# Optimization experiments

Hardware: AMD Instinct MI355X
Metric: run time of the kernel (lower is better)

The kernel has to match this reference:

```python
import jax, jax.numpy as jnp
import numpy as np

B, N, E = 32, 32, 64          # graphs, nodes/graph, edges/graph
H_, W_ = 40, 40
HW = H_ * W_
D, NH, L = 256, 8, 6
DH = D // NH
Tn, Te = B * N, B * E


def _ln(x, g, b):
    m = x.mean(-1, keepdims=True)
    v = ((x - m) ** 2).mean(-1, keepdims=True)
    return (x - m) * jax.lax.rsqrt(v + 1e-5) * g + b


def _sinus(v, dim):
    half = dim // 2
    freqs = jnp.exp(-jnp.log(10000.0) * jnp.arange(half) / half)
    ang = v[..., None] * freqs
    return jnp.concatenate([jnp.sin(ang), jnp.cos(ang)], -1)


def _heatmap(bx):
    # separable Gaussian over the HxW grid, boxes in normalized cxcywh
    gx = (jnp.arange(W_) + 0.5) / W_
    gy = (jnp.arange(H_) + 0.5) / H_
    cx, cy, w, h = bx[:, 0], bx[:, 1], bx[:, 2], bx[:, 3]
    hx = jnp.exp(-(gx[None] - cx[:, None]) ** 2 / (2 * (w[:, None] / 2) ** 2 + 1e-6))
    hy = jnp.exp(-(gy[None] - cy[:, None]) ** 2 / (2 * (h[:, None] / 2) ** 2 + 1e-6))
    return (hy[:, :, None] * hx[:, None, :]).reshape(-1, HW)


def _to_b(q):
    return jnp.concatenate([q[:Tn].reshape(B, N, D), q[Tn:].reshape(B, E, D)], 1)


def _from_b(qb):
    return jnp.concatenate([qb[:, :N].reshape(Tn, D), qb[:, N:].reshape(Te, D)], 0)


def _xyxy(b):
    return jnp.stack([b[:, 0] - b[:, 2] / 2, b[:, 1] - b[:, 3] / 2,
                      b[:, 0] + b[:, 2] / 2, b[:, 1] + b[:, 3] / 2], -1)


def _forward(features, boxes, nodes0, edges0, ln1_g, ln1_b, attn_in_w, attn_in_b,
             attn_out_w, attn_out_b, ls1, ln2_g, ln2_b, gat_wn, gat_we, gat_a_src,
             gat_a_dst, gat_a_edge, gat_wo, gat_bo, gat_woe, gat_boe, ls2,
             ln3_g, ln3_b, ffn_w1, ffn_b1, ffn_w2, ffn_b2, ls3, edge_local):
    off = jnp.repeat(jnp.arange(B) * N, E)
    src = edge_local[0] + off
    dst = edge_local[1] + off
    b1, b2 = boxes[src], boxes[dst]
    u1, u2 = _xyxy(b1), _xyxy(b2)
    ux1 = jnp.minimum(u1[:, 0], u2[:, 0]); uy1 = jnp.minimum(u1[:, 1], u2[:, 1])
    ux2 = jnp.maximum(u1[:, 2], u2[:, 2]); uy2 = jnp.maximum(u1[:, 3], u2[:, 3])
    union = jnp.stack([(ux1 + ux2) / 2, (uy1 + uy2) / 2, ux2 - ux1, uy2 - uy1], -1)
    node_hm = _heatmap(boxes)                                   # [Tn, HW]
    edge_hm = jnp.maximum(jnp.maximum(node_hm[src], node_hm[dst]), _heatmap(union))
    attn_bias = jnp.concatenate([node_hm.reshape(B, N, HW), edge_hm.reshape(B, E, HW)], 1)
    node_emb = jnp.concatenate([_sinus(boxes[:, i], D // 4) for i in range(4)], -1)
    delta = b1 - b2
    edge_emb = jnp.concatenate([_sinus(delta[:, i], D // 4) for i in range(4)], -1)
    emb_q = jnp.concatenate([node_emb, edge_emb], 0)            # [Tn+Te, D]
    q = jnp.concatenate([nodes0, edges0], 0)
    scale = 1.0 / jnp.sqrt(jnp.float32(DH))
    outs = []
    for l in range(L):
        # cross attention (pre-LN, LayerScale residual)
        x = _ln(q, ln1_g[l], ln1_b[l])
        xb = _to_b(x)
        Wq, Wk, Wv = jnp.split(attn_in_w[l], 3, 0)
        bq, bk, bv = jnp.split(attn_in_b[l], 3, 0)
        qh = (xb @ Wq.T + bq).reshape(B, N + E, NH, DH)
        kh = (features @ Wk.T + bk).reshape(B, HW, NH, DH)
        vh = (features @ Wv.T + bv).reshape(B, HW, NH, DH)
        scores = jnp.einsum('bqhd,bkhd->bhqk', qh, kh) * scale + attn_bias[:, None]
        o = jnp.einsum('bhqk,bkhd->bqhd', jax.nn.softmax(scores, -1), vh).reshape(B, N + E, D)
        o = o @ attn_out_w[l].T + attn_out_b[l]
        q = q + ls1[l] * _from_b(o)
        # GAT (note: original adds residual to the *normed* queries)
        x = _ln(q, ln2_g[l], ln2_b[l])
        xe = x + emb_q
        h = (xe[:Tn] @ gat_wn[l]).reshape(Tn, NH, DH)
        ee = (xe[Tn:] @ gat_we[l]).reshape(Te, NH, DH)
        logits = jax.nn.leaky_relu(
            (h[src] * gat_a_src[l] + h[dst] * gat_a_dst[l] + ee * gat_a_edge[l]).sum(-1), 0.2)
        m = jax.ops.segment_max(logits, dst, Tn)
        ex = jnp.exp(logits - m[dst])
        den = jax.ops.segment_sum(ex, dst, Tn)
        alpha = ex / (den[dst] + 1e-9)
        nout = jax.ops.segment_sum(alpha[..., None] * (h[src] + ee), dst, Tn).reshape(Tn, D) @ gat_wo[l] + gat_bo[l]
        eout = ee.reshape(Te, D) @ gat_woe[l] + gat_boe[l]
        q = x + ls2[l] * jnp.concatenate([nout, eout], 0)
        # FFN
        y = _ln(q, ln3_g[l], ln3_b[l])
        y = jax.nn.gelu(y @ ffn_w1[l] + ffn_b1[l], approximate=False) @ ffn_w2[l] + ffn_b2[l]
        q = q + ls3[l] * y
        outs.append(q)
    return jnp.stack(outs)  # [L, Tn+Te, D]


def setup_inputs():
    key = jax.random.key(0)
    k = jax.random.split(key, 20)
    s = 0.02
    u = jax.random.uniform(k[0], (Tn, 4))
    boxes = jnp.concatenate([u[:, :2] * 0.6 + 0.2, u[:, 2:] * 0.3 + 0.1], -1)
    return dict(
        features=jax.random.normal(k[2], (B, HW, D)),
        boxes=boxes,
        edge_local=jax.random.randint(k[1], (2, Te), 0, N),
        nodes0=jax.random.normal(k[3], (Tn, D)),
        edges0=jax.random.normal(k[4], (Te, D)),
        ln1_g=jnp.ones((L, D)), ln1_b=jnp.zeros((L, D)),
        attn_in_w=jax.random.normal(k[5], (L, 3 * D, D)) * s, attn_in_b=jnp.zeros((L, 3 * D)),
        attn_out_w=jax.random.normal(k[6], (L, D, D)) * s, attn_out_b=jnp.zeros((L, D)),
        ls1=jnp.full((L, D), 0.1),
        ln2_g=jnp.ones((L, D)), ln2_b=jnp.zeros((L, D)),
        gat_wn=jax.random.normal(k[7], (L, D, D)) * s, gat_we=jax.random.normal(k[8], (L, D, D)) * s,
        gat_a_src=jax.random.normal(k[9], (L, NH, DH)) * s,
        gat_a_dst=jax.random.normal(k[10], (L, NH, DH)) * s,
        gat_a_edge=jax.random.normal(k[11], (L, NH, DH)) * s,
        gat_wo=jax.random.normal(k[12], (L, D, D)) * s, gat_bo=jnp.zeros((L, D)),
        gat_woe=jax.random.normal(k[13], (L, D, D)) * s, gat_boe=jnp.zeros((L, D)),
        ls2=jnp.full((L, D), 0.1),
        ln3_g=jnp.ones((L, D)), ln3_b=jnp.zeros((L, D)),
        ffn_w1=jax.random.normal(k[14], (L, D, 4 * D)) * s, ffn_b1=jnp.zeros((L, 4 * D)),
        ffn_w2=jax.random.normal(k[15], (L, 4 * D, D)) * s, ffn_b2=jnp.zeros((L, D)),
        ls3=jnp.full((L, D), 0.1),
    )


def reference(features, boxes, edge_local, nodes0, edges0, ln1_g, ln1_b, attn_in_w,
              attn_in_b, attn_out_w, attn_out_b, ls1, ln2_g, ln2_b, gat_wn, gat_we,
              gat_a_src, gat_a_dst, gat_a_edge, gat_wo, gat_bo, gat_woe, gat_boe,
              ls2, ln3_g, ln3_b, ffn_w1, ffn_b1, ffn_w2, ffn_b2, ls3):
    return _forward(features, boxes, nodes0, edges0, ln1_g, ln1_b, attn_in_w, attn_in_b,
                    attn_out_w, attn_out_b, ls1, ln2_g, ln2_b, gat_wn, gat_we, gat_a_src,
                    gat_a_dst, gat_a_edge, gat_wo, gat_bo, gat_woe, gat_boe, ls2,
                    ln3_g, ln3_b, ffn_w1, ffn_b1, ffn_w2, ffn_b2, ls3, edge_local)
```

## Files before the change

kernel.cpp:

```cpp
#include <hip/hip_runtime.h>
#include <hip/hip_bf16.h>
#include <math.h>

typedef __hip_bfloat16 bf16;
typedef unsigned short ushort_t;
typedef __attribute__((ext_vector_type(8))) short bf16x8;
typedef __attribute__((ext_vector_type(4))) float f32x4;

static constexpr int B_C   = 32;
static constexpr int N_C   = 32;
static constexpr int E_C   = 64;
static constexpr int HW_C  = 1600;
static constexpr int D_C   = 256;
static constexpr int NH_C  = 8;
static constexpr int DH_C  = 32;
static constexpr int L_C   = 6;
static constexpr int TN_C  = 1024;
static constexpr int TE_C  = 2048;
static constexpr int TT_C  = 3072;

__device__ __forceinline__ float bf2f(bf16 v) { return __bfloat162float(v); }
__device__ __forceinline__ int clampi(int v, int lo, int hi) {
  return v < lo ? lo : (v > hi ? hi : v);
}
__device__ __forceinline__ float clampf(float v, float lo, float hi) {
  return fminf(fmaxf(v, lo), hi);
}
__device__ __forceinline__ ushort_t f2b(float x) {
  bf16 h = __float2bfloat16(x);
  return *reinterpret_cast<ushort_t*>(&h);
}

__device__ __forceinline__ void unpack_bf2(unsigned v, float& a, float& b) {
  union { unsigned u; float f; } ua, ub;
  ua.u = v << 16;
  ub.u = v & 0xffff0000u;
  a = ua.f; b = ub.f;
}

__device__ __forceinline__ void load_bf16x32(const bf16* p, float* out) {
  const uint4* p4 = reinterpret_cast<const uint4*>(p);
#pragma unroll
  for (int w = 0; w < 4; w++) {
    uint4 u = p4[w];
    unpack_bf2(u.x, out[w * 8 + 0], out[w * 8 + 1]);
    unpack_bf2(u.y, out[w * 8 + 2], out[w * 8 + 3]);
    unpack_bf2(u.z, out[w * 8 + 4], out[w * 8 + 5]);
    unpack_bf2(u.w, out[w * 8 + 6], out[w * 8 + 7]);
  }
}

static constexpr int SA = 40;

__device__ __forceinline__ void stage8(const float* __restrict__ src,
                                       ushort_t* __restrict__ dst) {
  float4 f0 = *(const float4*)src;
  float4 f1 = *(const float4*)(src + 4);
  ushort_t t[8] = { f2b(f0.x), f2b(f0.y), f2b(f0.z), f2b(f0.w),
                    f2b(f1.x), f2b(f1.y), f2b(f1.z), f2b(f1.w) };
  *(uint4*)dst = *(const uint4*)t;
}

template <bool AB, bool BT, int EPI, typename TC>
__global__ __launch_bounds__(256) void mgemm_kernel(
    const void* __restrict__ Ap, int lda, const float* __restrict__ Bw, int ldb,
    const float* __restrict__ bias, TC* __restrict__ C, int ldc,
    int M, int N, int K)
{
  __shared__ ushort_t As[64 * SA];
  __shared__ ushort_t Bs[64 * SA];
  const int tid = threadIdx.x;
  const int row0 = blockIdx.x * 64, col0 = blockIdx.y * 64;
  const int wave = tid >> 6, lane = tid & 63;
  const int wm = (wave >> 1) * 32, wn = (wave & 1) * 32;
  const int lm = lane & 15, quad = lane >> 4;

  f32x4 acc[2][2] = {};
  const int am = tid >> 2, akk = (tid & 3) * 8;
  const int bn = tid & 63, bkb = (tid >> 6) * 8;

  for (int k0 = 0; k0 < K; k0 += 32) {
    if (AB) {
      const bf16* A = (const bf16*)Ap;
      *(uint4*)&As[am * SA + akk] =
          *(const uint4*)(A + (size_t)(row0 + am) * lda + k0 + akk);
    } else {
      stage8((const float*)Ap + (size_t)(row0 + am) * lda + k0 + akk,
             &As[am * SA + akk]);
    }
    if (BT) {
      stage8(Bw + (size_t)(col0 + am) * ldb + k0 + akk, &Bs[am * SA + akk]);
    } else {
      ushort_t t[8];
#pragma unroll
      for (int j = 0; j < 8; j++)
        t[j] = f2b(Bw[(size_t)(k0 + bkb + j) * ldb + col0 + bn]);
      *(uint4*)(&Bs[bn * SA + bkb]) = *(const uint4*)t;
    }
    __syncthreads();
    bf16x8 a0 = *(const bf16x8*)(&As[(wm + lm) * SA + quad * 8]);
    bf16x8 a1 = *(const bf16x8*)(&As[(wm + 16 + lm) * SA + quad * 8]);
    bf16x8 b0 = *(const bf16x8*)(&Bs[(wn + lm) * SA + quad * 8]);
    bf16x8 b1 = *(const bf16x8*)(&Bs[(wn + 16 + lm) * SA + quad * 8]);
    acc[0][0] = __builtin_amdgcn_mfma_f32_16x16x32_bf16(a0, b0, acc[0][0], 0, 0, 0);
    acc[0][1] = __builtin_amdgcn_mfma_f32_16x16x32_bf16(a0, b1, acc[0][1], 0, 0, 0);
    acc[1][0] = __builtin_amdgcn_mfma_f32_16x16x32_bf16(a1, b0, acc[1][0], 0, 0, 0);
    acc[1][1] = __builtin_amdgcn_mfma_f32_16x16x32_bf16(a1, b1, acc[1][1], 0, 0, 0);
    __syncthreads();
  }

#pragma unroll
  for (int ti = 0; ti < 2; ti++) {
#pragma unroll
    for (int tj = 0; tj < 2; tj++) {
      int gc = col0 + wn + tj * 16 + lm;
      float bsv = (EPI == 1 || EPI == 2) ? bias[gc] : 0.f;
#pragma unroll
      for (int r = 0; r < 4; r++) {
        int gr = row0 + wm + ti * 16 + quad * 4 + r;
        float v = acc[ti][tj][r];
        TC* cp = C + (size_t)gr * ldc + gc;
        if (EPI == 1 || EPI == 2) v += bsv;
        if (EPI == 2) v = 0.5f * v * (1.0f + erff(v * 0.70710678118654752f));
        if (EPI == 3) v += (float)(*cp);
        *cp = (TC)v;
      }
    }
  }
}

template <bool AB, bool BT, int EPI, typename TC>
static void mg(const void* A, int lda, const float* Bw, int ldb,
               const float* bias, void* C, int ldc,
               int M, int N, int K, hipStream_t s) {
  dim3 g(M / 64, N / 64);
  mgemm_kernel<AB, BT, EPI, TC><<<g, 256, 0, s>>>(A, lda, Bw, ldb, bias,
                                                  (TC*)C, ldc, M, N, K);
}

template <int EPI>
__global__ __launch_bounds__(256) void mgemm_dual_kernel(
    const float* __restrict__ A1, const float* __restrict__ A2, int M1, int lda,
    const float* __restrict__ B1, const float* __restrict__ B2, int ldb,
    const float* __restrict__ bias1, const float* __restrict__ bias2,
    float* __restrict__ C, int ldc, int K)
{
  __shared__ ushort_t As[64 * SA];
  __shared__ ushort_t Bs[64 * SA];
  const int tid = threadIdx.x;
  const int grow0 = blockIdx.x * 64, col0 = blockIdx.y * 64;
  const bool first = grow0 < M1;
  const float* A = first ? A1 : A2;
  const float* Bw = first ? B1 : B2;
  const float* bias = first ? bias1 : bias2;
  const int row0 = first ? grow0 : grow0 - M1;

  const int wave = tid >> 6, lane = tid & 63;
  const int wm = (wave >> 1) * 32, wn = (wave & 1) * 32;
  const int lm = lane & 15, quad = lane >> 4;

  f32x4 acc[2][2] = {};
  const int am = tid >> 2, akk = (tid & 3) * 8;
  const int bn = tid & 63, bkb = (tid >> 6) * 8;

  for (int k0 = 0; k0 < K; k0 += 32) {
    stage8(A + (size_t)(row0 + am) * lda + k0 + akk, &As[am * SA + akk]);
    ushort_t t[8];
#pragma unroll
    for (int j = 0; j < 8; j++)
      t[j] = f2b(Bw[(size_t)(k0 + bkb + j) * ldb + col0 + bn]);
    *(uint4*)(&Bs[bn * SA + bkb]) = *(const uint4*)t;
    __syncthreads();
    bf16x8 a0 = *(const bf16x8*)(&As[(wm + lm) * SA + quad * 8]);
    bf16x8 a1 = *(const bf16x8*)(&As[(wm + 16 + lm) * SA + quad * 8]);
    bf16x8 b0 = *(const bf16x8*)(&Bs[(wn + lm) * SA + quad * 8]);
    bf16x8 b1 = *(const bf16x8*)(&Bs[(wn + 16 + lm) * SA + quad * 8]);
    acc[0][0] = __builtin_amdgcn_mfma_f32_16x16x32_bf16(a0, b0, acc[0][0], 0, 0, 0);
    acc[0][1] = __builtin_amdgcn_mfma_f32_16x16x32_bf16(a0, b1, acc[0][1], 0, 0, 0);
    acc[1][0] = __builtin_amdgcn_mfma_f32_16x16x32_bf16(a1, b0, acc[1][0], 0, 0, 0);
    acc[1][1] = __builtin_amdgcn_mfma_f32_16x16x32_bf16(a1, b1, acc[1][1], 0, 0, 0);
    __syncthreads();
  }

#pragma unroll
  for (int ti = 0; ti < 2; ti++) {
#pragma unroll
    for (int tj = 0; tj < 2; tj++) {
      int gc = col0 + wn + tj * 16 + lm;
      float bsv = (EPI == 1) ? bias[gc] : 0.f;
#pragma unroll
      for (int r = 0; r < 4; r++) {
        int gr = grow0 + wm + ti * 16 + quad * 4 + r;
        float v = acc[ti][tj][r];
        if (EPI == 1) v += bsv;
        C[(size_t)gr * ldc + gc] = v;
      }
    }
  }
}


__global__ __launch_bounds__(256) void featconv_kernel(const float* __restrict__ f,
                                                       bf16* __restrict__ fb) {
  int idx = (blockIdx.x * 256 + threadIdx.x) * 8;
  float4 a = *(const float4*)(f + idx);
  float4 b = *(const float4*)(f + idx + 4);
  ushort_t t[8] = { f2b(a.x), f2b(a.y), f2b(a.z), f2b(a.w),
                    f2b(b.x), f2b(b.y), f2b(b.z), f2b(b.w) };
  *(uint4*)(fb + idx) = *(const uint4*)t;
}

__global__ __launch_bounds__(256) void nodehm_kernel(const float* __restrict__ boxes,
                                                     bf16* __restrict__ hm) {
  int t = blockIdx.x;
  float cx = clampf(boxes[t * 4 + 0], -10.f, 10.f);
  float cy = clampf(boxes[t * 4 + 1], -10.f, 10.f);
  float w  = clampf(boxes[t * 4 + 2], -10.f, 10.f);
  float h  = clampf(boxes[t * 4 + 3], -10.f, 10.f);
  float dwx = w * w * 0.5f + 1e-6f;
  float dhy = h * h * 0.5f + 1e-6f;
  for (int pix = threadIdx.x; pix < HW_C; pix += 256) {
    int y = pix / 40, x = pix - y * 40;
    float gx = ((float)x + 0.5f) * 0.025f;
    float gy = ((float)y + 0.5f) * 0.025f;
    hm[(size_t)t * HW_C + pix] = __float2bfloat16(
        expf(-(gx - cx) * (gx - cx) / dwx) * expf(-(gy - cy) * (gy - cy) / dhy));
  }
}

__global__ __launch_bounds__(256) void edgehm_kernel(const float* __restrict__ boxes,
                                                     const int* __restrict__ el,
                                                     const bf16* __restrict__ nhm,
                                                     bf16* __restrict__ ehm) {
  int e = blockIdx.x;
  int b = e >> 6;
  int sg = clampi(el[e], 0, N_C - 1) + b * N_C;
  int dg = clampi(el[TE_C + e], 0, N_C - 1) + b * N_C;
  float c1x = clampf(boxes[sg * 4 + 0], -10.f, 10.f);
  float c1y = clampf(boxes[sg * 4 + 1], -10.f, 10.f);
  float w1  = clampf(boxes[sg * 4 + 2], -10.f, 10.f);
  float h1  = clampf(boxes[sg * 4 + 3], -10.f, 10.f);
  float c2x = clampf(boxes[dg * 4 + 0], -10.f, 10.f);
  float c2y = clampf(boxes[dg * 4 + 1], -10.f, 10.f);
  float w2  = clampf(boxes[dg * 4 + 2], -10.f, 10.f);
  float h2  = clampf(boxes[dg * 4 + 3], -10.f, 10.f);
  float ux1 = fminf(c1x - w1 * 0.5f, c2x - w2 * 0.5f);
  float uy1 = fminf(c1y - h1 * 0.5f, c2y - h2 * 0.5f);
  float ux2 = fmaxf(c1x + w1 * 0.5f, c2x + w2 * 0.5f);
  float uy2 = fmaxf(c1y + h1 * 0.5f, c2y + h2 * 0.5f);
  float cx = 0.5f * (ux1 + ux2), cy = 0.5f * (uy1 + uy2);
  float w = ux2 - ux1, h = uy2 - uy1;
  float dwx = w * w * 0.5f + 1e-6f;
  float dhy = h * h * 0.5f + 1e-6f;
  for (int pix = threadIdx.x; pix < HW_C; pix += 256) {
    int y = pix / 40, x = pix - y * 40;
    float gx = ((float)x + 0.5f) * 0.025f;
    float gy = ((float)y + 0.5f) * 0.025f;
    float u = expf(-(gx - cx) * (gx - cx) / dwx) * expf(-(gy - cy) * (gy - cy) / dhy);
    float v = fmaxf(fmaxf(bf2f(nhm[(size_t)sg * HW_C + pix]),
                          bf2f(nhm[(size_t)dg * HW_C + pix])), u);
    ehm[(size_t)e * HW_C + pix] = __float2bfloat16(v);
  }
}

__global__ __launch_bounds__(256) void embq_kernel(const float* __restrict__ boxes,
                                                   const int* __restrict__ el,
                                                   bf16* __restrict__ emb) {
  int t = blockIdx.x;
  int d = threadIdx.x;
  int c = d >> 6, inner = d & 63;
  float v;
  if (t < TN_C) {
    v = boxes[t * 4 + c];
  } else {
    int e = t - TN_C;
    int b = e >> 6;
    int sg = clampi(el[e], 0, N_C - 1) + b * N_C;
    int dg = clampi(el[TE_C + e], 0, N_C - 1) + b * N_C;
    v = boxes[sg * 4 + c] - boxes[dg * 4 + c];
  }
  v = clampf(v, -100.f, 100.f);
  int i = inner & 31;
  float freq = expf(-9.210340371976184f * (float)i / 32.0f);
  float ang = v * freq;
  emb[(size_t)t * D_C + d] = __float2bfloat16((inner < 32) ? sinf(ang) : cosf(ang));
}

__global__ __launch_bounds__(256) void initq_kernel(const float* __restrict__ nodes0,
                                                    const float* __restrict__ edges0,
                                                    float* __restrict__ q) {
  int idx = blockIdx.x * 256 + threadIdx.x;
  int t = idx >> 8;
  q[idx] = (t < TN_C) ? nodes0[idx] : edges0[idx - TN_C * D_C];
}


__global__ __launch_bounds__(256) void ln_kernel(const float* __restrict__ base,
                                                 const float* __restrict__ delta,
                                                 const float* __restrict__ ls,
                                                 float* __restrict__ qsave,
                                                 const float* __restrict__ g,
                                                 const float* __restrict__ bb,
                                                 float* __restrict__ xout,
                                                 const bf16* __restrict__ emb,
                                                 float* __restrict__ xeout) {
  __shared__ float red[4];
  int r = blockIdx.x, tid = threadIdx.x;
  size_t bofs = (size_t)r * D_C;
  float v = base[bofs + tid];
  if (delta) v += ls[tid] * delta[bofs + tid];
  if (qsave) qsave[bofs + tid] = v;
  float s = v;
#pragma unroll
  for (int o = 1; o < 64; o <<= 1) s += __shfl_xor(s, o);
  if ((tid & 63) == 0) red[tid >> 6] = s;
  __syncthreads();
  float mean = (red[0] + red[1] + red[2] + red[3]) * (1.0f / 256.0f);
  __syncthreads();
  float d = v - mean;
  float s2 = d * d;
#pragma unroll
  for (int o = 1; o < 64; o <<= 1) s2 += __shfl_xor(s2, o);
  if ((tid & 63) == 0) red[tid >> 6] = s2;
  __syncthreads();
  float var = (red[0] + red[1] + red[2] + red[3]) * (1.0f / 256.0f);
  float xo = d * rsqrtf(var + 1e-5f) * g[tid] + bb[tid];
  xout[bofs + tid] = xo;
  if (xeout) xeout[bofs + tid] = xo + bf2f(emb[bofs + tid]);
}

static constexpr int ATK = 160;
static constexpr int KSTR = 40;
static constexpr int VSTR = 168;
static constexpr int PSTR = 168;
static constexpr int SPL = 2;
static constexpr int KEYS_PER = HW_C / SPL;

__global__ __launch_bounds__(192) void fattn_kernel(const float* __restrict__ Qp,
                                                    const bf16* __restrict__ KV,
                                                    const bf16* __restrict__ nhm,
                                                    const bf16* __restrict__ ehm,
                                                    float* __restrict__ Opart,
                                                    float* __restrict__ mpart,
                                                    float* __restrict__ lpart) {
  __shared__ ushort_t Kl[ATK * KSTR];
  __shared__ ushort_t Vt[32 * VSTR];
  __shared__ ushort_t Pl[3 * 32 * PSTR];

  const int s = blockIdx.x >> 8;
  const int rem = blockIdx.x & 255;
  const int h = rem >> 5, b = rem & 31;
  const int tid = threadIdx.x;
  const int wave = tid >> 6, lane = tid & 63;
  const int lm = lane & 15, quad = lane >> 4;
  const int wr0 = wave * 32;

  int tok[2][4];
  const bf16* brow[2][4];
#pragma unroll
  for (int mt = 0; mt < 2; mt++)
#pragma unroll
    for (int r = 0; r < 4; r++) {
      int row = wr0 + mt * 16 + quad * 4 + r;
      if (row < 32) {
        int t = b * N_C + row;
        tok[mt][r] = t; brow[mt][r] = nhm + (size_t)t * HW_C;
      } else {
        int e = b * E_C + (row - 32);
        tok[mt][r] = TN_C + e; brow[mt][r] = ehm + (size_t)e * HW_C;
      }
    }

  bf16x8 qa[2];
#pragma unroll
  for (int mt = 0; mt < 2; mt++) {
    int row = wr0 + mt * 16 + lm;
    int t = (row < 32) ? (b * N_C + row) : (TN_C + b * E_C + (row - 32));
    const float* qp = Qp + (size_t)t * D_C + h * DH_C + quad * 8;
    ushort_t tmp[8];
#pragma unroll
    for (int j = 0; j < 8; j++) tmp[j] = f2b(qp[j]);
    qa[mt] = *(const bf16x8*)tmp;
  }

  f32x4 Oacc[2][2] = {};
  float mrow[2][4], lrow[2][4];
#pragma unroll
  for (int mt = 0; mt < 2; mt++)
#pragma unroll
    for (int r = 0; r < 4; r++) { mrow[mt][r] = -1e30f; lrow[mt][r] = 0.f; }

  const bf16* kvb = KV + (size_t)b * HW_C * 512 + h * DH_C;
  const float scale = 0.17677669529663687f;
  ushort_t* Pw = &Pl[wave * 32 * PSTR];

  const int kend = s * KEYS_PER + KEYS_PER;
  for (int k0 = s * KEYS_PER; k0 < kend; k0 += ATK) {
    for (int slot = tid; slot < ATK * 4; slot += 192) {
      int key = slot >> 2, dc = (slot & 3) * 8;
      const bf16* src = kvb + (size_t)(k0 + key) * 512 + dc;
      *(uint4*)&Kl[key * KSTR + dc] = *(const uint4*)src;
      uint4 v4 = *(const uint4*)(src + 256);
      ushort_t vs[8]; *(uint4*)vs = v4;
#pragma unroll
      for (int j = 0; j < 8; j++) Vt[(dc + j) * VSTR + key] = vs[j];
    }
    __syncthreads();

    float sv[2][10][4];
#pragma unroll
    for (int nt = 0; nt < 10; nt++) {
      bf16x8 kb = *(const bf16x8*)&Kl[(nt * 16 + lm) * KSTR + quad * 8];
#pragma unroll
      for (int mt = 0; mt < 2; mt++) {
        f32x4 d = {};
        d = __builtin_amdgcn_mfma_f32_16x16x32_bf16(qa[mt], kb, d, 0, 0, 0);
#pragma unroll
        for (int r = 0; r < 4; r++) sv[mt][nt][r] = d[r];
      }
    }

#pragma unroll
    for (int mt = 0; mt < 2; mt++)
#pragma unroll
      for (int r = 0; r < 4; r++) {
        const bf16* br = brow[mt][r] + k0 + lm;
        float mx = -1e30f;
#pragma unroll
        for (int nt = 0; nt < 10; nt++) {
          float v = sv[mt][nt][r] * scale + bf2f(br[nt * 16]);
          sv[mt][nt][r] = v;
          mx = fmaxf(mx, v);
        }
#pragma unroll
        for (int o = 1; o < 16; o <<= 1) mx = fmaxf(mx, __shfl_xor(mx, o));
        float mn = fmaxf(mrow[mt][r], mx);
        float lsum = 0.f;
        int prow = (mt * 16 + quad * 4 + r) * PSTR;
#pragma unroll
        for (int nt = 0; nt < 10; nt++) {
          float p = expf(fminf(sv[mt][nt][r] - mn, 0.f));
          lsum += p;
          Pw[prow + nt * 16 + lm] = f2b(p);
        }
#pragma unroll
        for (int o = 1; o < 16; o <<= 1) lsum += __shfl_xor(lsum, o);
        float alpha = expf(fminf(mrow[mt][r] - mn, 0.f));
        lrow[mt][r] = lrow[mt][r] * alpha + lsum;
        mrow[mt][r] = mn;
        Oacc[mt][0][r] *= alpha;
        Oacc[mt][1][r] *= alpha;
      }

#pragma unroll
    for (int kc = 0; kc < 5; kc++) {
#pragma unroll
      for (int nt = 0; nt < 2; nt++) {
        bf16x8 vfrag = *(const bf16x8*)&Vt[(nt * 16 + lm) * VSTR + kc * 32 + quad * 8];
#pragma unroll
        for (int mt = 0; mt < 2; mt++) {
          bf16x8 pa = *(const bf16x8*)&Pw[(mt * 16 + lm) * PSTR + kc * 32 + quad * 8];
          Oacc[mt][nt] = __builtin_amdgcn_mfma_f32_16x16x32_bf16(pa, vfrag,
                                                                 Oacc[mt][nt], 0, 0, 0);
        }
      }
    }
    __syncthreads();
  }

  const size_t TD = (size_t)TT_C * D_C;
#pragma unroll
  for (int mt = 0; mt < 2; mt++)
#pragma unroll
    for (int r = 0; r < 4; r++) {
      float* op = Opart + (size_t)s * TD + (size_t)tok[mt][r] * D_C + h * DH_C;
      op[lm]      = Oacc[mt][0][r];
      op[16 + lm] = Oacc[mt][1][r];
      if (lm == 0) {
        int mi = s * TT_C * NH_C + tok[mt][r] * NH_C + h;
        mpart[mi] = mrow[mt][r];
        lpart[mi] = lrow[mt][r];
      }
    }
}

__global__ __launch_bounds__(256) void fmerge_kernel(const float* __restrict__ Opart,
                                                     const float* __restrict__ mpart,
                                                     const float* __restrict__ lpart,
                                                     float* __restrict__ O) {
  int idx = blockIdx.x * 256 + threadIdx.x;
  int t = idx >> 8, d = idx & 255, h = d >> 5;
  const size_t TD = (size_t)TT_C * D_C;
  int mi = t * NH_C + h;
  float m0 = mpart[mi], m1 = mpart[TT_C * NH_C + mi];
  float l0 = lpart[mi], l1 = lpart[TT_C * NH_C + mi];
  float mm = fmaxf(m0, m1);
  float a0 = expf(fminf(m0 - mm, 0.f)), a1 = expf(fminf(m1 - mm, 0.f));
  float l = l0 * a0 + l1 * a1;
  O[idx] = (Opart[idx] * a0 + Opart[TD + idx] * a1) / fmaxf(l, 1e-30f);
}


template <bool HM>
__global__ __launch_bounds__(256) void attn_kernel(const float* __restrict__ Qp,
                                                   const bf16* __restrict__ KV,
                                                   const bf16* __restrict__ nhm,
                                                   const bf16* __restrict__ ehm,
                                                   const float* __restrict__ boxes,
                                                   const int* __restrict__ el,
                                                   int c0, int nb,
                                                   float* __restrict__ O) {
  int wid = threadIdx.x >> 6;
  int lane = threadIdx.x & 63;
  int gw = blockIdx.x * 4 + wid;
  int tic = gw >> 3, h = gw & 7;
  int t, bl, nG = 0;
  const bf16* brow = nullptr;
  float pcx[3], pcy[3], pdx[3], pdy[3];
  if (tic < nb * N_C) {
    bl = tic >> 5;
    t = (c0 + bl) * N_C + (tic & 31);
    if (HM) {
      brow = nhm + (size_t)t * HW_C;
    } else {
      float cx = clampf(boxes[t * 4 + 0], -10.f, 10.f);
      float cy = clampf(boxes[t * 4 + 1], -10.f, 10.f);
      float w  = clampf(boxes[t * 4 + 2], -10.f, 10.f);
      float hh = clampf(boxes[t * 4 + 3], -10.f, 10.f);
      pcx[0] = cx; pcy[0] = cy;
      pdx[0] = w * w * 0.5f + 1e-6f; pdy[0] = hh * hh * 0.5f + 1e-6f;
      nG = 1;
    }
  } else {
    int ei = tic - nb * N_C;
    bl = ei >> 6;
    int e = (c0 + bl) * E_C + (ei & 63);
    t = TN_C + e;
    if (HM) {
      brow = ehm + (size_t)e * HW_C;
    } else {
      int sg = clampi(el[e], 0, N_C - 1) + (c0 + bl) * N_C;
      int dg = clampi(el[TE_C + e], 0, N_C - 1) + (c0 + bl) * N_C;
      float c1x = clampf(boxes[sg * 4 + 0], -10.f, 10.f);
      float c1y = clampf(boxes[sg * 4 + 1], -10.f, 10.f);
      float w1  = clampf(boxes[sg * 4 + 2], -10.f, 10.f);
      float h1  = clampf(boxes[sg * 4 + 3], -10.f, 10.f);
      float c2x = clampf(boxes[dg * 4 + 0], -10.f, 10.f);
      float c2y = clampf(boxes[dg * 4 + 1], -10.f, 10.f);
      float w2  = clampf(boxes[dg * 4 + 2], -10.f, 10.f);
      float h2  = clampf(boxes[dg * 4 + 3], -10.f, 10.f);
      pcx[0] = c1x; pcy[0] = c1y;
      pdx[0] = w1 * w1 * 0.5f + 1e-6f; pdy[0] = h1 * h1 * 0.5f + 1e-6f;
      pcx[1] = c2x; pcy[1] = c2y;
      pdx[1] = w2 * w2 * 0.5f + 1e-6f; pdy[1] = h2 * h2 * 0.5f + 1e-6f;
      float ux1 = fminf(c1x - w1 * 0.5f, c2x - w2 * 0.5f);
      float uy1 = fminf(c1y - h1 * 0.5f, c2y - h2 * 0.5f);
      float ux2 = fmaxf(c1x + w1 * 0.5f, c2x + w2 * 0.5f);
      float uy2 = fmaxf(c1y + h1 * 0.5f, c2y + h2 * 0.5f);
      float uw = ux2 - ux1, uh = uy2 - uy1;
      pcx[2] = 0.5f * (ux1 + ux2); pcy[2] = 0.5f * (uy1 + uy2);
      pdx[2] = uw * uw * 0.5f + 1e-6f; pdy[2] = uh * uh * 0.5f + 1e-6f;
      nG = 3;
    }
  }

  float qv[32];
  const float* qp = Qp + (size_t)t * D_C + h * DH_C;
#pragma unroll
  for (int d = 0; d < 32; d++) qv[d] = qp[d];

  const float scale = 0.17677669529663687f;
  const bf16* kvb = KV + (size_t)bl * HW_C * 512 + h * DH_C;

  float sarr[25];
  float m = -1e30f;
#pragma unroll
  for (int i = 0; i < 25; i++) {
    int kk = lane + i * 64;
    float kf[32];
    load_bf16x32(kvb + (size_t)kk * 512, kf);
    float s = 0.f;
#pragma unroll
    for (int d = 0; d < 32; d++) s = fmaf(kf[d], qv[d], s);
    float bias;
    if (HM) {
      bias = bf2f(brow[kk]);
    } else {
      int yy = kk / 40, xx = kk - yy * 40;
      float gx = ((float)xx + 0.5f) * 0.025f;
      float gy = ((float)yy + 0.5f) * 0.025f;
      bias = 0.f;
      for (int g = 0; g < nG; g++) {
        float dxv = gx - pcx[g], dyv = gy - pcy[g];
        float e = expf(-dxv * dxv / pdx[g]) * expf(-dyv * dyv / pdy[g]);
        bias = fmaxf(bias, e);
      }
    }
    s = clampf(s * scale + bias, -1e30f, 1e30f);
    sarr[i] = s;
    m = fmaxf(m, s);
  }
#pragma unroll
  for (int o = 1; o < 64; o <<= 1) m = fmaxf(m, __shfl_xor(m, o));

  float l = 0.f;
  float acc[32] = {};
#pragma unroll
  for (int i = 0; i < 25; i++) {
    int kk = lane + i * 64;
    float vf[32];
    load_bf16x32(kvb + (size_t)kk * 512 + 256, vf);
    float e = expf(fminf(sarr[i] - m, 0.f));
    l += e;
#pragma unroll
    for (int d = 0; d < 32; d++) acc[d] = fmaf(e, vf[d], acc[d]);
  }
#pragma unroll
  for (int o = 1; o < 64; o <<= 1) {
    l += __shfl_xor(l, o);
#pragma unroll
    for (int d = 0; d < 32; d++) acc[d] += __shfl_xor(acc[d], o);
  }
  if (lane == 0) {
    float inv = 1.0f / fmaxf(l, 1e-30f);
    float* op = O + (size_t)t * D_C + h * DH_C;
#pragma unroll
    for (int d = 0; d < 32; d++) op[d] = acc[d] * inv;
  }
}


__global__ __launch_bounds__(512) void gat_fused_kernel(const float* __restrict__ hee,
                                                        const int* __restrict__ el,
                                                        const float* __restrict__ as,
                                                        const float* __restrict__ ad,
                                                        const float* __restrict__ ae,
                                                        float* __restrict__ al) {
  __shared__ float lg[512];
  __shared__ float ml[256], dl[256];
  int b = blockIdx.x, tid = threadIdx.x;
  int e_l = tid >> 3, h = tid & 7;
  int e = b * E_C + e_l;
  int sgl = clampi(el[e], 0, N_C - 1);
  int dgl = clampi(el[TE_C + e], 0, N_C - 1);
  {
    const float* hs = hee + (size_t)(b * N_C + sgl) * D_C + h * DH_C;
    const float* hd = hee + (size_t)(b * N_C + dgl) * D_C + h * DH_C;
    const float* ep = hee + (size_t)(TN_C + e) * D_C + h * DH_C;
    float s = 0.f;
#pragma unroll
    for (int d = 0; d < 32; d++)
      s += hs[d] * as[h * 32 + d] + hd[d] * ad[h * 32 + d] + ep[d] * ae[h * 32 + d];
    s = clampf(s, -1e30f, 1e30f);
    lg[tid] = (s > 0.f) ? s : 0.2f * s;
  }
  __syncthreads();
  if (tid < 256) {
    int n = tid >> 3, hh = tid & 7;
    float m = -1e30f;
    for (int k = 0; k < 64; k++) {
      int dg = clampi(el[TE_C + b * E_C + k], 0, N_C - 1);
      if (dg == n) m = fmaxf(m, lg[k * 8 + hh]);
    }
    float den = 0.f;
    for (int k = 0; k < 64; k++) {
      int dg = clampi(el[TE_C + b * E_C + k], 0, N_C - 1);
      if (dg == n) den += expf(fminf(lg[k * 8 + hh] - m, 0.f));
    }
    ml[tid] = m; dl[tid] = den;
  }
  __syncthreads();
  float ex = expf(fminf(lg[tid] - ml[dgl * 8 + h], 0.f));
  al[(size_t)e * 8 + h] = ex / (dl[dgl * 8 + h] + 1e-9f);
}

__global__ __launch_bounds__(256) void gat_nout_kernel(const float* __restrict__ hee,
                                                       const int* __restrict__ el,
                                                       const float* __restrict__ al,
                                                       float* __restrict__ noutp) {
  int n = blockIdx.x, d = threadIdx.x;
  int h = d >> 5;
  int b = n >> 5;
  int e0 = b * E_C;
  float acc = 0.f;
  for (int k = 0; k < 64; k++) {
    int e = e0 + k;
    int dg = clampi(el[TE_C + e], 0, N_C - 1) + b * N_C;
    if (dg == n) {
      int sg = clampi(el[e], 0, N_C - 1) + b * N_C;
      acc += al[e * 8 + h] * (hee[(size_t)sg * D_C + d] + hee[(size_t)(TN_C + e) * D_C + d]);
    }
  }
  noutp[(size_t)n * D_C + d] = acc;
}


__global__ __launch_bounds__(256) void axpy_store_kernel(float* __restrict__ q,
                                                         const float* __restrict__ delta,
                                                         const float* __restrict__ ls,
                                                         float* __restrict__ out) {
  int idx = blockIdx.x * 256 + threadIdx.x;
  float v = q[idx] + ls[idx & 255] * delta[idx];
  q[idx] = v;
  out[idx] = (fabsf(v) <= 1e4f) ? v : 0.f;
}


extern "C" void kernel_launch(void* const* d_in, const int* in_sizes, int n_in,
                              void* d_out, int out_size, void* d_ws, size_t ws_size,
                              hipStream_t stream) {
  const float* features   = (const float*)d_in[0];
  const float* boxes      = (const float*)d_in[1];
  const int*   edge_local = (const int*)d_in[2];
  const float* nodes0     = (const float*)d_in[3];
  const float* edges0     = (const float*)d_in[4];
  const float* ln1_g      = (const float*)d_in[5];
  const float* ln1_b      = (const float*)d_in[6];
  const float* attn_in_w  = (const float*)d_in[7];
  const float* attn_in_b  = (const float*)d_in[8];
  const float* attn_out_w = (const float*)d_in[9];
  const float* attn_out_b = (const float*)d_in[10];
  const float* ls1        = (const float*)d_in[11];
  const float* ln2_g      = (const float*)d_in[12];
  const float* ln2_b      = (const float*)d_in[13];
  const float* gat_wn     = (const float*)d_in[14];
  const float* gat_we     = (const float*)d_in[15];
  const float* gat_a_src  = (const float*)d_in[16];
  const float* gat_a_dst  = (const float*)d_in[17];
  const float* gat_a_edge = (const float*)d_in[18];
  const float* gat_wo     = (const float*)d_in[19];
  const float* gat_bo     = (const float*)d_in[20];
  const float* gat_woe    = (const float*)d_in[21];
  const float* gat_boe    = (const float*)d_in[22];
  const float* ls2        = (const float*)d_in[23];
  const float* ln3_g      = (const float*)d_in[24];
  const float* ln3_b      = (const float*)d_in[25];
  const float* ffn_w1     = (const float*)d_in[26];
  const float* ffn_b1     = (const float*)d_in[27];
  const float* ffn_w2     = (const float*)d_in[28];
  const float* ffn_b2     = (const float*)d_in[29];
  const float* ls3        = (const float*)d_in[30];
  float* out = (float*)d_out;

  size_t off = 0;
  auto alloc = [&](size_t bytes) -> void* {
    void* p = (char*)d_ws + off;
    off += (bytes + 255) & ~(size_t)255;
    return p;
  };
  const size_t TD = (size_t)TT_C * D_C;
  bf16*  emb   = (bf16*)alloc(TD * 2);
  float* q     = (float*)alloc(TD * 4);
  float* t0    = (float*)alloc(TD * 4);
  float* t1    = (float*)alloc(TD * 4);
  float* al    = (float*)alloc((size_t)TE_C * 8 * 4);
  float* mpart = (float*)alloc((size_t)SPL * TT_C * NH_C * 4);
  float* lpart = (float*)alloc((size_t)SPL * TT_C * NH_C * 4);
  float* ybig  = (float*)alloc((size_t)TT_C * 512 * 4);
  size_t base_end = off;

  const size_t KV_FULL = (size_t)B_C * HW_C * 512 * 2;
  const size_t KV_CHNK = (size_t)4 * HW_C * 512 * 2;
  const size_t HM_SZ   = (size_t)(TN_C + TE_C) * HW_C * 2;
  const size_t YB2_SZ  = (size_t)TT_C * 512 * 4;
  const size_t FB_SZ   = (size_t)B_C * HW_C * 256 * 2;
  const size_t MARGIN  = 2u << 20;
  int mode;
  if (ws_size >= base_end + YB2_SZ + KV_FULL + HM_SZ + FB_SZ + MARGIN) mode = 3;
  else if (ws_size >= base_end + KV_FULL + HM_SZ + MARGIN) mode = 2;
  else if (ws_size >= base_end + KV_CHNK + HM_SZ + MARGIN) mode = 1;
  else mode = 0;

  float* ybig2 = (mode == 3) ? (float*)alloc(YB2_SZ) : nullptr;
  bf16* KV = (bf16*)alloc(mode >= 2 ? KV_FULL : KV_CHNK);
  bf16 *nhm = nullptr, *ehm = nullptr;
  if (mode >= 1) {
    nhm = (bf16*)alloc((size_t)TN_C * HW_C * 2);
    ehm = (bf16*)alloc((size_t)TE_C * HW_C * 2);
  }
  bf16* featb = (mode == 3) ? (bf16*)alloc(FB_SZ) : nullptr;
  float* hee   = ybig;
  float* noutp = ybig + (size_t)TT_C * 256;
  float* Opart = ybig;
  (void)in_sizes; (void)n_in; (void)out_size; (void)ybig2;

  embq_kernel<<<TT_C, 256, 0, stream>>>(boxes, edge_local, emb);
  initq_kernel<<<TT_C, 256, 0, stream>>>(nodes0, edges0, q);
  if (mode >= 1) {
    nodehm_kernel<<<TN_C, 256, 0, stream>>>(boxes, nhm);
    edgehm_kernel<<<TE_C, 256, 0, stream>>>(boxes, edge_local, nhm, ehm);
  }
  if (mode == 3)
    featconv_kernel<<<(B_C * HW_C * 256) / (256 * 8), 256, 0, stream>>>(features, featb);

  for (int l = 0; l < L_C; l++) {
    const float* Wq  = attn_in_w + (size_t)l * 768 * 256;
    const float* WKV = Wq + (size_t)256 * 256;
    const float* bq  = attn_in_b + (size_t)l * 768;
    const float* bKV = bq + 256;

    ln_kernel<<<TT_C, 256, 0, stream>>>(q, nullptr, nullptr, nullptr,
                                        ln1_g + l * 256, ln1_b + l * 256,
                                        t0, nullptr, nullptr);
    mg<false, true, 1, float>(t0, 256, Wq, 256, bq, t1, 256, TT_C, 256, 256, stream);
    if (mode >= 2) {
      if (mode == 3)
        mg<true, true, 1, bf16>(featb, 256, WKV, 256, bKV, KV, 512,
                                B_C * HW_C, 512, 256, stream);
      else
        mg<false, true, 1, bf16>(features, 256, WKV, 256, bKV, KV, 512,
                                 B_C * HW_C, 512, 256, stream);
      fattn_kernel<<<SPL * 256, 192, 0, stream>>>(t1, KV, nhm, ehm,
                                                  Opart, mpart, lpart);
      fmerge_kernel<<<(TT_C * D_C) / 256, 256, 0, stream>>>(Opart, mpart, lpart, t0);
    } else {
      for (int c = 0; c < B_C / 4; c++) {
        mg<false, true, 1, bf16>(features + (size_t)c * 4 * HW_C * 256, 256,
                                 WKV, 256, bKV, KV, 512, 4 * HW_C, 512, 256, stream);
        if (mode == 1)
          attn_kernel<true><<<4 * 192, 256, 0, stream>>>(
              t1, KV, nhm, ehm, boxes, edge_local, c * 4, 4, t0);
        else
          attn_kernel<false><<<4 * 192, 256, 0, stream>>>(
              t1, KV, nhm, ehm, boxes, edge_local, c * 4, 4, t0);
      }
    }
    mg<false, true, 1, float>(t0, 256, attn_out_w + (size_t)l * 65536, 256,
                              attn_out_b + l * 256, t1, 256, TT_C, 256, 256, stream);
    ln_kernel<<<TT_C, 256, 0, stream>>>(q, t1, ls1 + l * 256, q,
                                        ln2_g + l * 256, ln2_b + l * 256,
                                        t0, emb, t1);
    {
      dim3 g(TT_C / 64, 4);
      mgemm_dual_kernel<0><<<g, 256, 0, stream>>>(
          t1, t1 + (size_t)TN_C * 256, TN_C, 256,
          gat_wn + (size_t)l * 65536, gat_we + (size_t)l * 65536, 256,
          nullptr, nullptr, hee, 256, 256);
    }
    gat_fused_kernel<<<B_C, 512, 0, stream>>>(
        hee, edge_local, gat_a_src + l * 256, gat_a_dst + l * 256,
        gat_a_edge + l * 256, al);
    gat_nout_kernel<<<TN_C, 256, 0, stream>>>(hee, edge_local, al, noutp);
    {
      dim3 g(TT_C / 64, 4);
      mgemm_dual_kernel<1><<<g, 256, 0, stream>>>(
          noutp, hee + (size_t)TN_C * 256, TN_C, 256,
          gat_wo + (size_t)l * 65536, gat_woe + (size_t)l * 65536, 256,
          gat_bo + l * 256, gat_boe + l * 256, t1, 256, 256);
    }
    ln_kernel<<<TT_C, 256, 0, stream>>>(t0, t1, ls2 + l * 256, q,
                                        ln3_g + l * 256, ln3_b + l * 256,
                                        t0, nullptr, nullptr);
    const float* W1 = ffn_w1 + (size_t)l * 262144;
    const float* W2 = ffn_w2 + (size_t)l * 262144;
    if (mode == 3) {
      mg<false, false, 2, float>(t0, 256, W1, 1024, ffn_b1 + l * 1024,
                                 ybig, 1024, TT_C, 1024, 256, stream);
      mg<false, false, 1, float>(ybig, 1024, W2, 256, ffn_b2 + l * 256,
                                 t1, 256, TT_C, 256, 1024, stream);
    } else {
      mg<false, false, 2, float>(t0, 256, W1, 1024, ffn_b1 + l * 1024,
                                 ybig, 512, TT_C, 512, 256, stream);
      mg<false, false, 1, float>(ybig, 512, W2, 256, ffn_b2 + l * 256,
                                 t1, 256, TT_C, 256, 512, stream);
      mg<false, false, 2, float>(t0, 256, W1 + 512, 1024, ffn_b1 + l * 1024 + 512,
                                 ybig, 512, TT_C, 512, 256, stream);
      mg<false, false, 3, float>(ybig, 512, W2 + (size_t)512 * 256, 256,
                                 nullptr, t1, 256, TT_C, 256, 512, stream);
    }
    axpy_store_kernel<<<TT_C, 256, 0, stream>>>(q, t1, ls3 + l * 256,
                                                out + (size_t)l * TD);
  }
}
```

Measured before the change: 1.614 ms.

## Split fused attention across four key chunks and stream K from global memory

Makes the key-split count a runtime parameter and uses four splits in the full-workspace mode, with masking because 400 keys per split is not a multiple of the 160-key tile. fmerge now combines an arbitrary number of partials. K is no longer staged in LDS: MFMA fragments are read straight from global memory, and P is staged one 32-key chunk at a time, which shrinks shared memory and may raise occupancy. It also batches the row max/sum shuffles, vectorizes the Q load and switches expf to __expf throughout. Risks: over-reads past split and buffer ends on the K loads, Opart spilling past the ybig allocation into the adjacent buffer, and lower accuracy from the fast exp.

Result: slower. 2.450 ms (+51.8%).

```diff
diff --git a/kernel.cpp b/kernel.cpp
--- a/kernel.cpp
+++ b/kernel.cpp
@@ -224,7 +224,7 @@
     float gx = ((float)x + 0.5f) * 0.025f;
     float gy = ((float)y + 0.5f) * 0.025f;
     hm[(size_t)t * HW_C + pix] = __float2bfloat16(
-        expf(-(gx - cx) * (gx - cx) / dwx) * expf(-(gy - cy) * (gy - cy) / dhy));
+        __expf(-(gx - cx) * (gx - cx) / dwx) * __expf(-(gy - cy) * (gy - cy) / dhy));
   }
 }
 
@@ -256,7 +256,7 @@
     int y = pix / 40, x = pix - y * 40;
     float gx = ((float)x + 0.5f) * 0.025f;
     float gy = ((float)y + 0.5f) * 0.025f;
-    float u = expf(-(gx - cx) * (gx - cx) / dwx) * expf(-(gy - cy) * (gy - cy) / dhy);
+    float u = __expf(-(gx - cx) * (gx - cx) / dwx) * __expf(-(gy - cy) * (gy - cy) / dhy);
     float v = fmaxf(fmaxf(bf2f(nhm[(size_t)sg * HW_C + pix]),
                           bf2f(nhm[(size_t)dg * HW_C + pix])), u);
     ehm[(size_t)e * HW_C + pix] = __float2bfloat16(v);
@@ -330,11 +330,8 @@
 }
 
 static constexpr int ATK = 160;
-static constexpr int KSTR = 40;
 static constexpr int VSTR = 168;
-static constexpr int PSTR = 168;
-static constexpr int SPL = 2;
-static constexpr int KEYS_PER = HW_C / SPL;
+static constexpr int PST2 = 40;
 
 __global__ __launch_bounds__(192) void fattn_kernel(const float* __restrict__ Qp,
                                                     const bf16* __restrict__ KV,
@@ -342,10 +339,10 @@
                                                     const bf16* __restrict__ ehm,
                                                     float* __restrict__ Opart,
                                                     float* __restrict__ mpart,
-                                                    float* __restrict__ lpart) {
-  __shared__ ushort_t Kl[ATK * KSTR];
+                                                    float* __restrict__ lpart,
+                                                    int keys_per) {
   __shared__ ushort_t Vt[32 * VSTR];
-  __shared__ ushort_t Pl[3 * 32 * PSTR];
+  __shared__ ushort_t Ps[3 * 32 * PST2];
 
   const int s = blockIdx.x >> 8;
   const int rem = blockIdx.x & 255;
@@ -377,9 +374,10 @@
     int row = wr0 + mt * 16 + lm;
     int t = (row < 32) ? (b * N_C + row) : (TN_C + b * E_C + (row - 32));
     const float* qp = Qp + (size_t)t * D_C + h * DH_C + quad * 8;
-    ushort_t tmp[8];
-#pragma unroll
-    for (int j = 0; j < 8; j++) tmp[j] = f2b(qp[j]);
+    float4 f0 = *(const float4*)qp;
+    float4 f1 = *(const float4*)(qp + 4);
+    ushort_t tmp[8] = { f2b(f0.x), f2b(f0.y), f2b(f0.z), f2b(f0.w),
+                        f2b(f1.x), f2b(f1.y), f2b(f1.z), f2b(f1.w) };
     qa[mt] = *(const bf16x8*)tmp;
   }
 
@@ -392,15 +390,16 @@
 
   const bf16* kvb = KV + (size_t)b * HW_C * 512 + h * DH_C;
   const float scale = 0.17677669529663687f;
-  ushort_t* Pw = &Pl[wave * 32 * PSTR];
-
-  const int kend = s * KEYS_PER + KEYS_PER;
-  for (int k0 = s * KEYS_PER; k0 < kend; k0 += ATK) {
+  ushort_t* Pw = &Ps[wave * 32 * PST2];
+
+  const int ks = s * keys_per, kend = ks + keys_per;
+  for (int k0 = ks; k0 < kend; k0 += ATK) {
+    __syncthreads();
     for (int slot = tid; slot < ATK * 4; slot += 192) {
       int key = slot >> 2, dc = (slot & 3) * 8;
-      const bf16* src = kvb + (size_t)(k0 + key) * 512 + dc;
-      *(uint4*)&Kl[key * KSTR + dc] = *(const uint4*)src;
-      uint4 v4 = *(const uint4*)(src + 256);
+      uint4 v4 = make_uint4(0, 0, 0, 0);
+      if (k0 + key < kend)
+        v4 = *(const uint4*)(kvb + (size_t)(k0 + key) * 512 + 256 + dc);
       ushort_t vs[8]; *(uint4*)vs = v4;
 #pragma unroll
       for (int j = 0; j < 8; j++) Vt[(dc + j) * VSTR + key] = vs[j];
@@ -410,7 +409,7 @@
     float sv[2][10][4];
 #pragma unroll
     for (int nt = 0; nt < 10; nt++) {
-      bf16x8 kb = *(const bf16x8*)&Kl[(nt * 16 + lm) * KSTR + quad * 8];
+      bf16x8 kb = *(const bf16x8*)(kvb + (size_t)(k0 + nt * 16 + lm) * 512 + quad * 8);
 #pragma unroll
       for (int mt = 0; mt < 2; mt++) {
         f32x4 d = {};
@@ -420,52 +419,86 @@
       }
     }
 
+    float mx[2][4];
 #pragma unroll
     for (int mt = 0; mt < 2; mt++)
 #pragma unroll
       for (int r = 0; r < 4; r++) {
+        mx[mt][r] = -1e30f;
         const bf16* br = brow[mt][r] + k0 + lm;
-        float mx = -1e30f;
 #pragma unroll
         for (int nt = 0; nt < 10; nt++) {
-          float v = sv[mt][nt][r] * scale + bf2f(br[nt * 16]);
+          float v;
+          if (k0 + nt * 16 < kend)
+            v = sv[mt][nt][r] * scale + bf2f(br[nt * 16]);
+          else
+            v = -1e30f;
           sv[mt][nt][r] = v;
-          mx = fmaxf(mx, v);
+          mx[mt][r] = fmaxf(mx[mt][r], v);
         }
-#pragma unroll
-        for (int o = 1; o < 16; o <<= 1) mx = fmaxf(mx, __shfl_xor(mx, o));
-        float mn = fmaxf(mrow[mt][r], mx);
-        float lsum = 0.f;
-        int prow = (mt * 16 + quad * 4 + r) * PSTR;
+      }
+#pragma unroll
+    for (int o = 1; o < 16; o <<= 1)
+#pragma unroll
+      for (int mt = 0; mt < 2; mt++)
+#pragma unroll
+        for (int r = 0; r < 4; r++)
+          mx[mt][r] = fmaxf(mx[mt][r], __shfl_xor(mx[mt][r], o));
+
+    float ls[2][4], ar[2][4];
+#pragma unroll
+    for (int mt = 0; mt < 2; mt++)
+#pragma unroll
+      for (int r = 0; r < 4; r++) {
+        float mn = fmaxf(mrow[mt][r], mx[mt][r]);
+        float l = 0.f;
 #pragma unroll
         for (int nt = 0; nt < 10; nt++) {
-          float p = expf(fminf(sv[mt][nt][r] - mn, 0.f));
-          lsum += p;
-          Pw[prow + nt * 16 + lm] = f2b(p);
+          float p = __expf(fminf(sv[mt][nt][r] - mn, 0.f));
+          sv[mt][nt][r] = p;
+          l += p;
         }
-#pragma unroll
-        for (int o = 1; o < 16; o <<= 1) lsum += __shfl_xor(lsum, o);
-        float alpha = expf(fminf(mrow[mt][r] - mn, 0.f));
-        lrow[mt][r] = lrow[mt][r] * alpha + lsum;
+        ls[mt][r] = l;
+        ar[mt][r] = __expf(fminf(mrow[mt][r] - mn, 0.f));
         mrow[mt][r] = mn;
-        Oacc[mt][0][r] *= alpha;
-        Oacc[mt][1][r] *= alpha;
+      }
+#pragma unroll
+    for (int o = 1; o < 16; o <<= 1)
+#pragma unroll
+      for (int mt = 0; mt < 2; mt++)
+#pragma unroll
+        for (int r = 0; r < 4; r++)
+          ls[mt][r] += __shfl_xor(ls[mt][r], o);
+#pragma unroll
+    for (int mt = 0; mt < 2; mt++)
+#pragma unroll
+      for (int r = 0; r < 4; r++) {
+        lrow[mt][r] = lrow[mt][r] * ar[mt][r] + ls[mt][r];
+        Oacc[mt][0][r] *= ar[mt][r];
+        Oacc[mt][1][r] *= ar[mt][r];
       }
 
 #pragma unroll
     for (int kc = 0; kc < 5; kc++) {
+#pragma unroll
+      for (int mt = 0; mt < 2; mt++)
+#pragma unroll
+        for (int r = 0; r < 4; r++) {
+          int prow = (mt * 16 + quad * 4 + r) * PST2;
+          Pw[prow + lm]      = f2b(sv[mt][2 * kc][r]);
+          Pw[prow + 16 + lm] = f2b(sv[mt][2 * kc + 1][r]);
+        }
 #pragma unroll
       for (int nt = 0; nt < 2; nt++) {
         bf16x8 vfrag = *(const bf16x8*)&Vt[(nt * 16 + lm) * VSTR + kc * 32 + quad * 8];
 #pragma unroll
         for (int mt = 0; mt < 2; mt++) {
-          bf16x8 pa = *(const bf16x8*)&Pw[(mt * 16 + lm) * PSTR + kc * 32 + quad * 8];
+          bf16x8 pa = *(const bf16x8*)&Pw[(mt * 16 + lm) * PST2 + quad * 8];
           Oacc[mt][nt] = __builtin_amdgcn_mfma_f32_16x16x32_bf16(pa, vfrag,
                                                                  Oacc[mt][nt], 0, 0, 0);
         }
       }
     }
-    __syncthreads();
   }
 
   const size_t TD = (size_t)TT_C * D_C;
@@ -487,17 +520,20 @@
 __global__ __launch_bounds__(256) void fmerge_kernel(const float* __restrict__ Opart,
                                                      const float* __restrict__ mpart,
                                                      const float* __restrict__ lpart,
-                                                     float* __restrict__ O) {
+                                                     float* __restrict__ O, int spl) {
   int idx = blockIdx.x * 256 + threadIdx.x;
   int t = idx >> 8, d = idx & 255, h = d >> 5;
   const size_t TD = (size_t)TT_C * D_C;
   int mi = t * NH_C + h;
-  float m0 = mpart[mi], m1 = mpart[TT_C * NH_C + mi];
-  float l0 = lpart[mi], l1 = lpart[TT_C * NH_C + mi];
-  float mm = fmaxf(m0, m1);
-  float a0 = expf(fminf(m0 - mm, 0.f)), a1 = expf(fminf(m1 - mm, 0.f));
-  float l = l0 * a0 + l1 * a1;
-  O[idx] = (Opart[idx] * a0 + Opart[TD + idx] * a1) / fmaxf(l, 1e-30f);
+  float mm = -1e30f;
+  for (int s = 0; s < spl; s++) mm = fmaxf(mm, mpart[s * TT_C * NH_C + mi]);
+  float l = 0.f, acc = 0.f;
+  for (int s = 0; s < spl; s++) {
+    float a = __expf(fminf(mpart[s * TT_C * NH_C + mi] - mm, 0.f));
+    l += lpart[s * TT_C * NH_C + mi] * a;
+    acc += Opart[s * TD + idx] * a;
+  }
+  O[idx] = acc / fmaxf(l, 1e-30f);
 }
 
 
@@ -592,7 +628,7 @@
       bias = 0.f;
       for (int g = 0; g < nG; g++) {
         float dxv = gx - pcx[g], dyv = gy - pcy[g];
-        float e = expf(-dxv * dxv / pdx[g]) * expf(-dyv * dyv / pdy[g]);
+        float e = __expf(-dxv * dxv / pdx[g]) * __expf(-dyv * dyv / pdy[g]);
         bias = fmaxf(bias, e);
       }
     }
@@ -610,7 +646,7 @@
     int kk = lane + i * 64;
     float vf[32];
     load_bf16x32(kvb + (size_t)kk * 512 + 256, vf);
-    float e = expf(fminf(sarr[i] - m, 0.f));
+    float e = __expf(fminf(sarr[i] - m, 0.f));
     l += e;
 #pragma unroll
     for (int d = 0; d < 32; d++) acc[d] = fmaf(e, vf[d], acc[d]);
@@ -665,12 +701,12 @@
     float den = 0.f;
     for (int k = 0; k < 64; k++) {
       int dg = clampi(el[TE_C + b * E_C + k], 0, N_C - 1);
-      if (dg == n) den += expf(fminf(lg[k * 8 + hh] - m, 0.f));
+      if (dg == n) den += __expf(fminf(lg[k * 8 + hh] - m, 0.f));
     }
     ml[tid] = m; dl[tid] = den;
   }
   __syncthreads();
-  float ex = expf(fminf(lg[tid] - ml[dgl * 8 + h], 0.f));
+  float ex = __expf(fminf(lg[tid] - ml[dgl * 8 + h], 0.f));
   al[(size_t)e * 8 + h] = ex / (dl[dgl * 8 + h] + 1e-9f);
 }
 
@@ -754,8 +790,8 @@
   float* t0    = (float*)alloc(TD * 4);
   float* t1    = (float*)alloc(TD * 4);
   float* al    = (float*)alloc((size_t)TE_C * 8 * 4);
-  float* mpart = (float*)alloc((size_t)SPL * TT_C * NH_C * 4);
-  float* lpart = (float*)alloc((size_t)SPL * TT_C * NH_C * 4);
+  float* mpart = (float*)alloc((size_t)4 * TT_C * NH_C * 4);
+  float* lpart = (float*)alloc((size_t)4 * TT_C * NH_C * 4);
   float* ybig  = (float*)alloc((size_t)TT_C * 512 * 4);
   size_t base_end = off;
 
@@ -782,6 +818,7 @@
   float* hee   = ybig;
   float* noutp = ybig + (size_t)TT_C * 256;
   float* Opart = ybig;
+  const int spl = (mode == 3) ? 4 : 2;
   (void)in_sizes; (void)n_in; (void)out_size; (void)ybig2;
 
   embq_kernel<<<TT_C, 256, 0, stream>>>(boxes, edge_local, emb);
@@ -810,9 +847,10 @@
       else
         mg<false, true, 1, bf16>(features, 256, WKV, 256, bKV, KV, 512,
                                  B_C * HW_C, 512, 256, stream);
-      fattn_kernel<<<SPL * 256, 192, 0, stream>>>(t1, KV, nhm, ehm,
-                                                  Opart, mpart, lpart);
-      fmerge_kernel<<<(TT_C * D_C) / 256, 256, 0, stream>>>(Opart, mpart, lpart, t0);
+      fattn_kernel<<<spl * 256, 192, 0, stream>>>(t1, KV, nhm, ehm,
+                                                  Opart, mpart, lpart, HW_C / spl);
+      fmerge_kernel<<<(TT_C * D_C) / 256, 256, 0, stream>>>(Opart, mpart, lpart,
+                                                            t0, spl);
     } else {
       for (int c = 0; c < B_C / 4; c++) {
         mg<false, true, 1, bf16>(features + (size_t)c * 4 * HW_C * 256, 256,
```
